# Kernel optimization log

Measured on AMD Instinct MI355X. Metric: run time of the kernel, lower is better.

Reference implementation:

```python
import jax, jax.numpy as jnp
import numpy as np

T, B, E, H = 256, 8, 512, 32
EXP = 512            # number of expanded (periodic-image) keys
SMOOTH = 20.0        # smooth_factor


def setup_inputs() -> dict:
    key = jax.random.key(0)
    ks = jax.random.split(key, 12)
    s = 1.0 / np.sqrt(E)
    return {
        "query": jax.random.normal(ks[0], (T, B, E), dtype=jnp.float32),
        "outcell_index": jax.random.randint(ks[1], (B, EXP), 0, T),
        "expand_mask": jax.random.bernoulli(ks[2], 0.1, (B, EXP)),
        "key_padding_mask": jax.random.bernoulli(ks[3], 0.1, (B, T)),
        "local_attention_weight": jax.random.uniform(ks[4], (B, T, T + EXP), dtype=jnp.float32),
        "Wq": jax.random.normal(ks[5], (E, E), dtype=jnp.float32) * s,
        "bq": jnp.zeros((E,), dtype=jnp.float32),
        "Wk": jax.random.normal(ks[6], (E, E), dtype=jnp.float32) * s,   # k_bias=False
        "Wv": jax.random.normal(ks[7], (E, E), dtype=jnp.float32) * s,
        "bv": jnp.zeros((E,), dtype=jnp.float32),
        "Wo": jax.random.normal(ks[8], (E, E), dtype=jnp.float32) * s,
        "bo": jnp.zeros((E,), dtype=jnp.float32),
    }


def reference(query, outcell_index, expand_mask, key_padding_mask,
              local_attention_weight, Wq, bq, Wk, Wv, bv, Wo, bo):
    t, b, e = query.shape
    hd = e // H
    # QKV projections (torch Linear: y = x @ W.T + b)
    q = jnp.einsum('tbe,fe->tbf', query, Wq) + bq
    k = jnp.einsum('tbe,fe->tbf', query, Wk)          # no k bias
    v = jnp.einsum('tbe,fe->tbf', query, Wv) + bv
    # PBC gather-expand K/V along the time axis
    oc = outcell_index.T[:, :, None]                  # [EXP, B, 1]
    k = jnp.concatenate([k, jnp.take_along_axis(k, oc, axis=0)], axis=0)  # [S,B,E]
    v = jnp.concatenate([v, jnp.take_along_axis(v, oc, axis=0)], axis=0)
    s_len = k.shape[0]
    # [len, B, E] -> [B, H, len, hd]
    qh = q.reshape(t, b, H, hd).transpose(1, 2, 0, 3)
    kh = k.reshape(s_len, b, H, hd).transpose(1, 2, 0, 3)
    vh = v.reshape(s_len, b, H, hd).transpose(1, 2, 0, 3)
    # NOTE: forward() never applies self.scaling in this path (faithful)
    scores = jnp.einsum('bhtd,bhsd->bhts', qh, kh)    # [B,H,T,S]
    law = local_attention_weight[:, None]             # [B,1,T,S]
    scores = (scores + SMOOTH) * law - SMOOTH         # smooth softmax
    kpm = jnp.concatenate([key_padding_mask, expand_mask], axis=1)  # [B,S]
    scores = jnp.where(kpm[:, None, None, :], -jnp.inf, scores)
    probs = jax.nn.softmax(scores, axis=-1)
    probs = probs * law                               # post-softmax reweight
    attn = jnp.einsum('bhts,bhsd->bhtd', probs, vh)   # [B,H,T,hd]
    attn = attn.transpose(2, 0, 1, 3).reshape(t, b, e)
    return jnp.einsum('tbe,fe->tbf', attn, Wo) + bo
```

## Files before the change

### kernel.cpp

```cpp
#include <hip/hip_runtime.h>
#include <stdint.h>

#define T_ 256
#define B_ 8
#define E_ 512
#define H_ 32
#define HD_ 16
#define EXP_ 512
#define S_ 768
#define M_ 2048
#define SMOOTH_ 20.0f
#define PSTR 40
#define VSTR 800
#define LOG2E_ 1.44269504f
#define MB0_  (-100.988655f)

typedef __attribute__((ext_vector_type(8)))  short bf16x8;
typedef __attribute__((ext_vector_type(4)))  float f32x4;
typedef __attribute__((ext_vector_type(16))) float f32x16;

__device__ __forceinline__ unsigned int pku(float a, float b)
{
    return ((__float_as_uint(a) + 0x8000u) >> 16) |
           ((__float_as_uint(b) + 0x8000u) & 0xFFFF0000u);
}
__device__ __forceinline__ ushort bf1(float a)
{
    unsigned int u = __float_as_uint(a);
    u = u + 0x7FFFu + ((u >> 16) & 1u);
    return (ushort)(u >> 16);
}

union U16 { uint4 u; bf16x8 v; };

__global__ __launch_bounds__(512, 4)
void qkv_attn_kernel(const float* __restrict__ X,
                     const float* __restrict__ Wq, const float* __restrict__ Wk,
                     const float* __restrict__ Wv,
                     const float* __restrict__ bq, const float* __restrict__ bv,
                     const float* __restrict__ LAW,
                     const int* __restrict__ kpm, const int* __restrict__ em,
                     const int* __restrict__ oc, ushort* __restrict__ Ab)
{
    __shared__ __align__(16) char raw[81920];
    ushort* Ks  = (ushort*)(raw);
    ushort* Vt  = (ushort*)(raw + 24576);
    ushort* Qi  = (ushort*)(raw + 50176);
    float*  msf = (float*) (raw + 58368);
    ushort* Pbb = (ushort*)(raw + 61440);
    ushort* As  = (ushort*)(raw);
    ushort* Bs  = (ushort*)(raw + 36864);
    ushort* Ob  = Qi;

    const int bh  = blockIdx.x;
    const int b   = bh >> 5;
    const int h   = bh & 31;
    const int tid = threadIdx.x;
    const int w   = tid >> 6;
    const int l   = tid & 63;

    const int r0 = tid >> 3;
    const int c8 = tid & 7;
    const float* Xc = &X[((size_t)r0 * 8 + b) * E_ + c8 * 8];

    const int wr = tid >> 3;
    const int wk = tid & 7;
    const float* Wsel = (wr < 16) ? Wq : (wr < 32 ? Wk : Wv);
    const float* Wr = &Wsel[((size_t)(h * 16 + (wr & 15))) * E_ + wk * 8];
    const bool wload = (tid < 384);

    ushort* Bxw = &Bs[wr * 72 + wk * 8];

    f32x4 acc[2][3];
#pragma unroll
    for (int i = 0; i < 2; ++i)
#pragma unroll
        for (int m = 0; m < 3; ++m)
            acc[i][m] = (f32x4){0.f, 0.f, 0.f, 0.f};

    float4 xp[4][2], wp[2];
#pragma unroll
    for (int k = 0; k < 4; ++k) {
        xp[k][0] = *(const float4*)&Xc[(size_t)k * 262144];
        xp[k][1] = *(const float4*)&Xc[(size_t)k * 262144 + 4];
    }
    if (wload) { wp[0] = *(const float4*)&Wr[0]; wp[1] = *(const float4*)&Wr[4]; }

    const int ln = l & 15;
    const int lg = l >> 4;

    for (int it = 0; it < 8; ++it) {
        __syncthreads();
#pragma unroll
        for (int k = 0; k < 4; ++k)
            *(uint4*)&As[(r0 + 64 * k) * 72 + c8 * 8] = make_uint4(
                pku(xp[k][0].x, xp[k][0].y), pku(xp[k][0].z, xp[k][0].w),
                pku(xp[k][1].x, xp[k][1].y), pku(xp[k][1].z, xp[k][1].w));
        if (wload)
            *(uint4*)&Bxw[0] = make_uint4(pku(wp[0].x, wp[0].y), pku(wp[0].z, wp[0].w),
                                          pku(wp[1].x, wp[1].y), pku(wp[1].z, wp[1].w));
        __syncthreads();
        if (it < 7) {
            Xc += 64;
#pragma unroll
            for (int k = 0; k < 4; ++k) {
                xp[k][0] = *(const float4*)&Xc[(size_t)k * 262144];
                xp[k][1] = *(const float4*)&Xc[(size_t)k * 262144 + 4];
            }
            if (wload) { Wr += 64; wp[0] = *(const float4*)&Wr[0]; wp[1] = *(const float4*)&Wr[4]; }
        }
#pragma unroll
        for (int kb = 0; kb < 2; ++kb) {
            bf16x8 af0 = *(const bf16x8*)&As[(32 * w + ln) * 72 + kb * 32 + lg * 8];
            bf16x8 af1 = *(const bf16x8*)&As[(32 * w + 16 + ln) * 72 + kb * 32 + lg * 8];
#pragma unroll
            for (int m = 0; m < 3; ++m) {
                bf16x8 bfm = *(const bf16x8*)&Bs[(m * 16 + ln) * 72 + kb * 32 + lg * 8];
                acc[0][m] = __builtin_amdgcn_mfma_f32_16x16x32_bf16(af0, bfm, acc[0][m], 0, 0, 0);
                acc[1][m] = __builtin_amdgcn_mfma_f32_16x16x32_bf16(af1, bfm, acc[1][m], 0, 0, 0);
            }
        }
    }

    __syncthreads();

    {
        const float bqv = bq[h * 16 + ln];
        const float bvv = bv[h * 16 + ln];
#pragma unroll
        for (int i = 0; i < 2; ++i)
#pragma unroll
            for (int r = 0; r < 4; ++r) {
                const int t = 32 * w + 16 * i + lg * 4 + r;
                Qi[t * 16 + ln]    = bf1(acc[i][0][r] + bqv);
                Ks[t * 16 + ln]    = bf1(acc[i][1][r]);
                Vt[ln * VSTR + t]  = bf1(acc[i][2][r] + bvv);
            }
    }
    __syncthreads();

    {
        const int j   = tid;
        const int src = oc[b * EXP_ + j];
        uint4 k0 = *(const uint4*)&Ks[src * 16];
        uint4 k1 = *(const uint4*)&Ks[src * 16 + 8];
        *(uint4*)&Ks[(T_ + j) * 16]     = k0;
        *(uint4*)&Ks[(T_ + j) * 16 + 8] = k1;
#pragma unroll
        for (int d = 0; d < 16; ++d)
            Vt[d * VSTR + T_ + j] = Vt[d * VSTR + src];

        const int s = tid;
        const int m = (s < T_) ? kpm[b * T_ + s] : em[b * EXP_ + (s - T_)];
        msf[s] = m ? -1.0e5f : MB0_;
        if (tid < 256) {
            const int s2 = 512 + tid;
            msf[s2] = em[b * EXP_ + (s2 - T_)] ? -1.0e5f : MB0_;
        }
    }
    __syncthreads();

    const int slane = l & 31;
    const int khalf = l >> 5;
    const int tl = l & 15;
    const int kg = l >> 4;

    bf16x8 qf = *(const bf16x8*)&Qi[(w * 32 + slane) * 16 + khalf * 8];

    const f32x16 zero16 = {0.f,0.f,0.f,0.f,0.f,0.f,0.f,0.f,
                           0.f,0.f,0.f,0.f,0.f,0.f,0.f,0.f};
    f32x4 o0 = {0.f, 0.f, 0.f, 0.f};
    f32x4 o1 = {0.f, 0.f, 0.f, 0.f};
    float zacc[16];
#pragma unroll
    for (int r = 0; r < 16; ++r) zacc[r] = 0.f;

    const float* lawb = &LAW[((size_t)b * T_ + w * 32 + khalf * 4) * S_ + slane];
    ushort* pw = &Pbb[w * 32 * PSTR + slane];
    ushort* pt = &Pbb[w * 32 * PSTR];
    float*  Zbw = (float*)pt;

    for (int i = 0; i < S_ / 32; ++i) {
        bf16x8 kf = *(const bf16x8*)&Ks[(i * 32 + slane) * 16 + khalf * 8];

        float lw[16];
        const float* lp = lawb + i * 32;
#pragma unroll
        for (int r = 0; r < 16; ++r)
            lw[r] = lp[(size_t)((r & 3) + 8 * (r >> 2)) * S_];

        f32x16 sc = __builtin_amdgcn_mfma_f32_32x32x16_bf16(qf, kf, zero16, 0, 0, 0);
        const float mb = msf[i * 32 + slane];

#pragma unroll
        for (int r = 0; r < 16; ++r) {
            const float lwK = lw[r] * LOG2E_;
            const float arg = __builtin_fmaf(sc[r], lwK,
                              __builtin_fmaf(lwK, SMOOTH_, mb));
            const float e = __builtin_amdgcn_exp2f(arg);
            zacc[r] += e;
            const float p = e * lw[r];
            pw[((r & 3) + 8 * (r >> 2) + 4 * khalf) * PSTR] =
                (ushort)((__float_as_uint(p) + 0x8000u) >> 16);
        }

        bf16x8 vf = *(const bf16x8*)&Vt[tl * VSTR + i * 32 + kg * 8];
        {
            const ushort* pr0 = &pt[(0 * 16 + tl) * PSTR + kg * 8];
            U16 u;
            uint2 a0 = *(const uint2*)pr0;
            uint2 a1 = *(const uint2*)(pr0 + 4);
            u.u = make_uint4(a0.x, a0.y, a1.x, a1.y);
            o0 = __builtin_amdgcn_mfma_f32_16x16x32_bf16(vf, u.v, o0, 0, 0, 0);
            const ushort* pr1 = &pt[(1 * 16 + tl) * PSTR + kg * 8];
            uint2 b0 = *(const uint2*)pr1;
            uint2 b1 = *(const uint2*)(pr1 + 4);
            u.u = make_uint4(b0.x, b0.y, b1.x, b1.y);
            o1 = __builtin_amdgcn_mfma_f32_16x16x32_bf16(vf, u.v, o1, 0, 0, 0);
        }
    }

#pragma unroll
    for (int m = 1; m < 32; m <<= 1) {
#pragma unroll
        for (int r = 0; r < 16; ++r)
            zacc[r] += __shfl_xor(zacc[r], m);
    }
    if (l == 0 || l == 32) {
#pragma unroll
        for (int r = 0; r < 16; ++r)
            Zbw[(r & 3) + 8 * (r >> 2) + 4 * khalf] = zacc[r];
    }
    __syncthreads();

#pragma unroll
    for (int th = 0; th < 2; ++th) {
        const int trow = th * 16 + tl;
        const float Zt  = Zbw[trow];
        const float inv = (Zt > 0.f) ? 1.f / Zt : 0.f;
        const f32x4 o = th ? o1 : o0;
        const int t = w * 32 + trow;
        *(uint*)&Ob[t * 16 + kg * 4]     = pku(o[0] * inv, o[1] * inv);
        *(uint*)&Ob[t * 16 + kg * 4 + 2] = pku(o[2] * inv, o[3] * inv);
    }
    __syncthreads();

    {
        ushort* dp = &Ab[((size_t)(b * H_ + h)) * T_ * HD_];
        *(uint4*)&dp[tid * 8] = *(const uint4*)&Ob[tid * 8];
    }
}

__device__ __forceinline__ void out_gemm_body(const ushort* __restrict__ Xh, int xstep,
                                              const float* __restrict__ Wf, int wstep,
                                              f32x4 acc[2][2],
                                              ushort* As, ushort* Bs)
{
    const int tid  = threadIdx.x;
    const int lrow = tid >> 2;
    const int kq   = tid & 3;
    const int l    = tid & 63;
    const int w    = tid >> 6;
    const int wm   = w & 1;
    const int wn   = w >> 1;
    const int lq   = l >> 4;
    const int ln   = l & 15;

    ushort* Aw = &As[lrow * 72 + kq * 16];
    ushort* Bw = &Bs[lrow * 72 + kq * 16];

    uint4  ha0 = *(const uint4*)&Xh[0];
    uint4  ha1 = *(const uint4*)&Xh[8];
    float4 fb0 = *(const float4*)&Wf[0];
    float4 fb1 = *(const float4*)&Wf[4];
    float4 fb2 = *(const float4*)&Wf[8];
    float4 fb3 = *(const float4*)&Wf[12];

    for (int it = 0; it < E_ / 64; ++it) {
        __syncthreads();
        *(uint4*)&Aw[0] = ha0;
        *(uint4*)&Aw[8] = ha1;
        *(uint4*)&Bw[0] = make_uint4(pku(fb0.x, fb0.y), pku(fb0.z, fb0.w),
                                     pku(fb1.x, fb1.y), pku(fb1.z, fb1.w));
        *(uint4*)&Bw[8] = make_uint4(pku(fb2.x, fb2.y), pku(fb2.z, fb2.w),
                                     pku(fb3.x, fb3.y), pku(fb3.z, fb3.w));
        __syncthreads();
        if (it < E_ / 64 - 1) {
            Xh += xstep;
            ha0 = *(const uint4*)&Xh[0];
            ha1 = *(const uint4*)&Xh[8];
            Wf += wstep;
            fb0 = *(const float4*)&Wf[0];
            fb1 = *(const float4*)&Wf[4];
            fb2 = *(const float4*)&Wf[8];
            fb3 = *(const float4*)&Wf[12];
        }
#pragma unroll
        for (int kb = 0; kb < 2; ++kb) {
            bf16x8 af0 = *(const bf16x8*)&As[(32 * wm + ln) * 72 + 32 * kb + lq * 8];
            bf16x8 af1 = *(const bf16x8*)&As[(32 * wm + 16 + ln) * 72 + 32 * kb + lq * 8];
            bf16x8 bf0 = *(const bf16x8*)&Bs[(32 * wn + ln) * 72 + 32 * kb + lq * 8];
            bf16x8 bf1 = *(const bf16x8*)&Bs[(32 * wn + 16 + ln) * 72 + 32 * kb + lq * 8];
            acc[0][0] = __builtin_amdgcn_mfma_f32_16x16x32_bf16(af0, bf0, acc[0][0], 0, 0, 0);
            acc[0][1] = __builtin_amdgcn_mfma_f32_16x16x32_bf16(af0, bf1, acc[0][1], 0, 0, 0);
            acc[1][0] = __builtin_amdgcn_mfma_f32_16x16x32_bf16(af1, bf0, acc[1][0], 0, 0, 0);
            acc[1][1] = __builtin_amdgcn_mfma_f32_16x16x32_bf16(af1, bf1, acc[1][1], 0, 0, 0);
        }
    }
}

__global__ __launch_bounds__(256)
void out_gemm(const ushort* __restrict__ Ab, const float* __restrict__ Wo,
              const float* __restrict__ bo, float* __restrict__ dst)
{
    __shared__ __align__(16) ushort AsBs[2 * 64 * 72];
    ushort* As = AsBs;
    ushort* Bs = AsBs + 64 * 72;

    const int m0 = blockIdx.y * 64;
    const int n0 = blockIdx.x * 64;

    f32x4 acc[2][2];
#pragma unroll
    for (int i = 0; i < 2; ++i)
#pragma unroll
        for (int j = 0; j < 2; ++j)
            acc[i][j] = (f32x4){0.f, 0.f, 0.f, 0.f};

    const int tid  = threadIdx.x;
    const int lrow = tid >> 2;
    const int kq   = tid & 3;
    const int m    = m0 + lrow;
    const int t    = m >> 3;
    const int b    = m & 7;
    out_gemm_body(&Ab[(((size_t)(b * H_ + kq)) * T_ + t) * HD_], 4 * T_ * HD_,
                  &Wo[(size_t)(n0 + lrow) * E_ + kq * 16], 64,
                  acc, As, Bs);

    const int l  = tid & 63;
    const int w  = tid >> 6;
    const int wm = w & 1;
    const int wn = w >> 1;
    const int lq = l >> 4;
    const int ln = l & 15;

    const float bo0 = bo[n0 + 32 * wn + ln];
    const float bo1 = bo[n0 + 32 * wn + 16 + ln];

    __syncthreads();
    float* Lf = (float*)AsBs;
#pragma unroll
    for (int j = 0; j < 2; ++j) {
        const float bb = j ? bo1 : bo0;
#pragma unroll
        for (int i = 0; i < 2; ++i)
#pragma unroll
            for (int r = 0; r < 4; ++r)
                Lf[(32 * wm + 16 * i + lq * 4 + r) * 68 + 32 * wn + 16 * j + ln] =
                    acc[i][j][r] + bb;
    }
    __syncthreads();

    {
        const int lm = tid & 63;
        const int hh = tid >> 6;
        float* dp = &dst[(size_t)(m0 + lm) * E_ + n0 + hh * 16];
#pragma unroll
        for (int c = 0; c < 4; ++c) {
            float4 v = *(const float4*)&Lf[lm * 68 + hh * 16 + c * 4];
            *(float4*)&dp[c * 4] = v;
        }
    }
}

extern "C" void kernel_launch(void* const* d_in, const int* in_sizes, int n_in,
                              void* d_out, int out_size, void* d_ws, size_t ws_size,
                              hipStream_t stream)
{
    const float* query = (const float*)d_in[0];
    const int*   oc    = (const int*)d_in[1];
    const int*   em    = (const int*)d_in[2];
    const int*   kpm   = (const int*)d_in[3];
    const float* law   = (const float*)d_in[4];
    const float* Wq    = (const float*)d_in[5];
    const float* bq    = (const float*)d_in[6];
    const float* Wk    = (const float*)d_in[7];
    const float* Wv    = (const float*)d_in[8];
    const float* bv    = (const float*)d_in[9];
    const float* Wo    = (const float*)d_in[10];
    const float* bo    = (const float*)d_in[11];
    float* out = (float*)d_out;

    ushort* Ab = (ushort*)d_ws;

    qkv_attn_kernel<<<B_ * H_, 512, 0, stream>>>(query, Wq, Wk, Wv, bq, bv,
                                                 law, kpm, em, oc, Ab);

    dim3 go(E_ / 64, M_ / 64, 1);
    out_gemm<<<go, 256, 0, stream>>>(Ab, Wo, bo, out);
}
```

Measured before the change: 129.1 us.

## Double attention block to 1024 threads, split key range and reduce partials

The fused QKV+attention kernel now launches 1024 threads per (batch, head). The projection gives each wave 16 rows, and the attention loop is split so two groups of waves each cover half of the 768 keys. Their partial outputs and softmax denominators are combined through LDS. The intermediate attention buffer is also written in [t,b,e] row-major layout, so the output GEMM reads contiguous rows instead of strided per-head chunks. This adds latency hiding and parallelism at the cost of more LDS (100KB), an extra reduction sync, and lower occupancy.

```diff
diff --git a/kernel.cpp b/kernel.cpp
--- a/kernel.cpp
+++ b/kernel.cpp
@@ -12,6 +12,7 @@
 #define SMOOTH_ 20.0f
 #define PSTR 40
 #define VSTR 800
+#define OSTR 20
 #define LOG2E_ 1.44269504f
 #define MB0_  (-100.988655f)
 
@@ -33,7 +34,7 @@
 
 union U16 { uint4 u; bf16x8 v; };
 
-__global__ __launch_bounds__(512, 4)
+__global__ __launch_bounds__(1024, 4)
 void qkv_attn_kernel(const float* __restrict__ X,
                      const float* __restrict__ Wq, const float* __restrict__ Wk,
                      const float* __restrict__ Wv,
@@ -42,7 +43,7 @@
                      const int* __restrict__ kpm, const int* __restrict__ em,
                      const int* __restrict__ oc, ushort* __restrict__ Ab)
 {
-    __shared__ __align__(16) char raw[81920];
+    __shared__ __align__(16) char raw[102400];
     ushort* Ks  = (ushort*)(raw);
     ushort* Vt  = (ushort*)(raw + 24576);
     ushort* Qi  = (ushort*)(raw + 50176);
@@ -50,6 +51,8 @@
     ushort* Pbb = (ushort*)(raw + 61440);
     ushort* As  = (ushort*)(raw);
     ushort* Bs  = (ushort*)(raw + 36864);
+    float*  Obuf= (float*) (raw);
+    float*  Zb  = (float*) (raw + 58368);
     ushort* Ob  = Qi;
 
     const int bh  = blockIdx.x;
@@ -61,63 +64,52 @@
 
     const int r0 = tid >> 3;
     const int c8 = tid & 7;
-    const float* Xc = &X[((size_t)r0 * 8 + b) * E_ + c8 * 8];
+    const float* Xc0 = &X[((size_t)r0 * 8 + b) * E_ + c8 * 8];
+    const float* Xc1 = Xc0 + (size_t)128 * 8 * E_;
 
     const int wr = tid >> 3;
-    const int wk = tid & 7;
+    const bool wload = (tid < 384);
     const float* Wsel = (wr < 16) ? Wq : (wr < 32 ? Wk : Wv);
-    const float* Wr = &Wsel[((size_t)(h * 16 + (wr & 15))) * E_ + wk * 8];
-    const bool wload = (tid < 384);
-
-    ushort* Bxw = &Bs[wr * 72 + wk * 8];
-
-    f32x4 acc[2][3];
-#pragma unroll
-    for (int i = 0; i < 2; ++i)
-#pragma unroll
-        for (int m = 0; m < 3; ++m)
-            acc[i][m] = (f32x4){0.f, 0.f, 0.f, 0.f};
-
-    float4 xp[4][2], wp[2];
-#pragma unroll
-    for (int k = 0; k < 4; ++k) {
-        xp[k][0] = *(const float4*)&Xc[(size_t)k * 262144];
-        xp[k][1] = *(const float4*)&Xc[(size_t)k * 262144 + 4];
-    }
-    if (wload) { wp[0] = *(const float4*)&Wr[0]; wp[1] = *(const float4*)&Wr[4]; }
+    const float* Wr = &Wsel[((size_t)(h * 16 + (wr & 15))) * E_ + c8 * 8];
+    ushort* Bxw = &Bs[wr * 72 + c8 * 8];
+
+    f32x4 acc[3];
+#pragma unroll
+    for (int m = 0; m < 3; ++m) acc[m] = (f32x4){0.f, 0.f, 0.f, 0.f};
+
+    float4 xa0, xa1, xb0, xb1, wp0, wp1;
+    xa0 = *(const float4*)&Xc0[0]; xa1 = *(const float4*)&Xc0[4];
+    xb0 = *(const float4*)&Xc1[0]; xb1 = *(const float4*)&Xc1[4];
+    if (wload) { wp0 = *(const float4*)&Wr[0]; wp1 = *(const float4*)&Wr[4]; }
 
     const int ln = l & 15;
     const int lg = l >> 4;
 
     for (int it = 0; it < 8; ++it) {
         __syncthreads();
-#pragma unroll
-        for (int k = 0; k < 4; ++k)
-            *(uint4*)&As[(r0 + 64 * k) * 72 + c8 * 8] = make_uint4(
-                pku(xp[k][0].x, xp[k][0].y), pku(xp[k][0].z, xp[k][0].w),
-                pku(xp[k][1].x, xp[k][1].y), pku(xp[k][1].z, xp[k][1].w));
+        *(uint4*)&As[r0 * 72 + c8 * 8] =
+            make_uint4(pku(xa0.x, xa0.y), pku(xa0.z, xa0.w),
+                       pku(xa1.x, xa1.y), pku(xa1.z, xa1.w));
+        *(uint4*)&As[(r0 + 128) * 72 + c8 * 8] =
+            make_uint4(pku(xb0.x, xb0.y), pku(xb0.z, xb0.w),
+                       pku(xb1.x, xb1.y), pku(xb1.z, xb1.w));
         if (wload)
-            *(uint4*)&Bxw[0] = make_uint4(pku(wp[0].x, wp[0].y), pku(wp[0].z, wp[0].w),
-                                          pku(wp[1].x, wp[1].y), pku(wp[1].z, wp[1].w));
+            *(uint4*)&Bxw[0] = make_uint4(pku(wp0.x, wp0.y), pku(wp0.z, wp0.w),
+                                          pku(wp1.x, wp1.y), pku(wp1.z, wp1.w));
         __syncthreads();
         if (it < 7) {
-            Xc += 64;
-#pragma unroll
-            for (int k = 0; k < 4; ++k) {
-                xp[k][0] = *(const float4*)&Xc[(size_t)k * 262144];
-                xp[k][1] = *(const float4*)&Xc[(size_t)k * 262144 + 4];
-            }
-            if (wload) { Wr += 64; wp[0] = *(const float4*)&Wr[0]; wp[1] = *(const float4*)&Wr[4]; }
+            Xc0 += 64; Xc1 += 64;
+            xa0 = *(const float4*)&Xc0[0]; xa1 = *(const float4*)&Xc0[4];
+            xb0 = *(const float4*)&Xc1[0]; xb1 = *(const float4*)&Xc1[4];
+            if (wload) { Wr += 64; wp0 = *(const float4*)&Wr[0]; wp1 = *(const float4*)&Wr[4]; }
         }
 #pragma unroll
         for (int kb = 0; kb < 2; ++kb) {
-            bf16x8 af0 = *(const bf16x8*)&As[(32 * w + ln) * 72 + kb * 32 + lg * 8];
-            bf16x8 af1 = *(const bf16x8*)&As[(32 * w + 16 + ln) * 72 + kb * 32 + lg * 8];
+            bf16x8 af = *(const bf16x8*)&As[(w * 16 + ln) * 72 + kb * 32 + lg * 8];
 #pragma unroll
             for (int m = 0; m < 3; ++m) {
                 bf16x8 bfm = *(const bf16x8*)&Bs[(m * 16 + ln) * 72 + kb * 32 + lg * 8];
-                acc[0][m] = __builtin_amdgcn_mfma_f32_16x16x32_bf16(af0, bfm, acc[0][m], 0, 0, 0);
-                acc[1][m] = __builtin_amdgcn_mfma_f32_16x16x32_bf16(af1, bfm, acc[1][m], 0, 0, 0);
+                acc[m] = __builtin_amdgcn_mfma_f32_16x16x32_bf16(af, bfm, acc[m], 0, 0, 0);
             }
         }
     }
@@ -128,35 +120,33 @@
         const float bqv = bq[h * 16 + ln];
         const float bvv = bv[h * 16 + ln];
 #pragma unroll
-        for (int i = 0; i < 2; ++i)
-#pragma unroll
-            for (int r = 0; r < 4; ++r) {
-                const int t = 32 * w + 16 * i + lg * 4 + r;
-                Qi[t * 16 + ln]    = bf1(acc[i][0][r] + bqv);
-                Ks[t * 16 + ln]    = bf1(acc[i][1][r]);
-                Vt[ln * VSTR + t]  = bf1(acc[i][2][r] + bvv);
-            }
-    }
-    __syncthreads();
-
-    {
+        for (int r = 0; r < 4; ++r) {
+            const int t = w * 16 + lg * 4 + r;
+            Qi[t * 16 + ln]   = bf1(acc[0][r] + bqv);
+            Ks[t * 16 + ln]   = bf1(acc[1][r]);
+            Vt[ln * VSTR + t] = bf1(acc[2][r] + bvv);
+        }
+    }
+    __syncthreads();
+
+    if (tid < 512) {
         const int j   = tid;
         const int src = oc[b * EXP_ + j];
         uint4 k0 = *(const uint4*)&Ks[src * 16];
         uint4 k1 = *(const uint4*)&Ks[src * 16 + 8];
         *(uint4*)&Ks[(T_ + j) * 16]     = k0;
         *(uint4*)&Ks[(T_ + j) * 16 + 8] = k1;
+    } else {
+        const int j   = tid - 512;
+        const int src = oc[b * EXP_ + j];
 #pragma unroll
         for (int d = 0; d < 16; ++d)
             Vt[d * VSTR + T_ + j] = Vt[d * VSTR + src];
-
+    }
+    if (tid < 768) {
         const int s = tid;
         const int m = (s < T_) ? kpm[b * T_ + s] : em[b * EXP_ + (s - T_)];
         msf[s] = m ? -1.0e5f : MB0_;
-        if (tid < 256) {
-            const int s2 = 512 + tid;
-            msf[s2] = em[b * EXP_ + (s2 - T_)] ? -1.0e5f : MB0_;
-        }
     }
     __syncthreads();
 
@@ -164,8 +154,10 @@
     const int khalf = l >> 5;
     const int tl = l & 15;
     const int kg = l >> 4;
-
-    bf16x8 qf = *(const bf16x8*)&Qi[(w * 32 + slane) * 16 + khalf * 8];
+    const int tq = w & 7;
+    const int sh = w >> 3;
+
+    bf16x8 qf = *(const bf16x8*)&Qi[(tq * 32 + slane) * 16 + khalf * 8];
 
     const f32x16 zero16 = {0.f,0.f,0.f,0.f,0.f,0.f,0.f,0.f,
                            0.f,0.f,0.f,0.f,0.f,0.f,0.f,0.f};
@@ -175,12 +167,11 @@
 #pragma unroll
     for (int r = 0; r < 16; ++r) zacc[r] = 0.f;
 
-    const float* lawb = &LAW[((size_t)b * T_ + w * 32 + khalf * 4) * S_ + slane];
+    const float* lawb = &LAW[((size_t)b * T_ + tq * 32 + khalf * 4) * S_ + slane];
     ushort* pw = &Pbb[w * 32 * PSTR + slane];
     ushort* pt = &Pbb[w * 32 * PSTR];
-    float*  Zbw = (float*)pt;
-
-    for (int i = 0; i < S_ / 32; ++i) {
+
+    for (int i = sh * 12; i < sh * 12 + 12; ++i) {
         bf16x8 kf = *(const bf16x8*)&Ks[(i * 32 + slane) * 16 + khalf * 8];
 
         float lw[16];
@@ -226,33 +217,50 @@
         for (int r = 0; r < 16; ++r)
             zacc[r] += __shfl_xor(zacc[r], m);
     }
+
+    __syncthreads();
+
     if (l == 0 || l == 32) {
 #pragma unroll
         for (int r = 0; r < 16; ++r)
-            Zbw[(r & 3) + 8 * (r >> 2) + 4 * khalf] = zacc[r];
-    }
-    __syncthreads();
-
-#pragma unroll
-    for (int th = 0; th < 2; ++th) {
-        const int trow = th * 16 + tl;
-        const float Zt  = Zbw[trow];
-        const float inv = (Zt > 0.f) ? 1.f / Zt : 0.f;
-        const f32x4 o = th ? o1 : o0;
-        const int t = w * 32 + trow;
-        *(uint*)&Ob[t * 16 + kg * 4]     = pku(o[0] * inv, o[1] * inv);
-        *(uint*)&Ob[t * 16 + kg * 4 + 2] = pku(o[2] * inv, o[3] * inv);
+            Zb[sh * 256 + tq * 32 + (r & 3) + 8 * (r >> 2) + 4 * khalf] = zacc[r];
+    }
+    if (sh == 1) {
+#pragma unroll
+        for (int th = 0; th < 2; ++th) {
+            const f32x4 o = th ? o1 : o0;
+            *(float4*)&Obuf[((size_t)(tq * 32 + th * 16 + tl)) * OSTR + kg * 4] =
+                make_float4(o[0], o[1], o[2], o[3]);
+        }
+    }
+    __syncthreads();
+
+    if (sh == 0) {
+#pragma unroll
+        for (int th = 0; th < 2; ++th) {
+            const int t = tq * 32 + th * 16 + tl;
+            const float Zt  = Zb[t] + Zb[256 + t];
+            const float inv = (Zt > 0.f) ? 1.f / Zt : 0.f;
+            float4 po = *(const float4*)&Obuf[(size_t)t * OSTR + kg * 4];
+            const f32x4 o = th ? o1 : o0;
+            float ov[4] = {(o[0] + po.x) * inv, (o[1] + po.y) * inv,
+                           (o[2] + po.z) * inv, (o[3] + po.w) * inv};
+            *(uint*)&Ob[t * 16 + kg * 4]     = pku(ov[0], ov[1]);
+            *(uint*)&Ob[t * 16 + kg * 4 + 2] = pku(ov[2], ov[3]);
+        }
     }
     __syncthreads();
 
     {
-        ushort* dp = &Ab[((size_t)(b * H_ + h)) * T_ * HD_];
-        *(uint4*)&dp[tid * 8] = *(const uint4*)&Ob[tid * 8];
-    }
-}
-
-__device__ __forceinline__ void out_gemm_body(const ushort* __restrict__ Xh, int xstep,
-                                              const float* __restrict__ Wf, int wstep,
+        const int t  = tid >> 2;
+        const int q4 = tid & 3;
+        *(uint2*)&Ab[((size_t)(t * 8 + b)) * E_ + h * 16 + q4 * 4] =
+            *(const uint2*)&Ob[t * 16 + q4 * 4];
+    }
+}
+
+__device__ __forceinline__ void out_gemm_body(const ushort* __restrict__ Xh,
+                                              const float* __restrict__ Wf,
                                               f32x4 acc[2][2],
                                               ushort* As, ushort* Bs)
 {
@@ -286,10 +294,10 @@
                                      pku(fb3.x, fb3.y), pku(fb3.z, fb3.w));
         __syncthreads();
         if (it < E_ / 64 - 1) {
-            Xh += xstep;
+            Xh += 64;
             ha0 = *(const uint4*)&Xh[0];
             ha1 = *(const uint4*)&Xh[8];
-            Wf += wstep;
+            Wf += 64;
             fb0 = *(const float4*)&Wf[0];
             fb1 = *(const float4*)&Wf[4];
             fb2 = *(const float4*)&Wf[8];
@@ -330,11 +338,8 @@
     const int tid  = threadIdx.x;
     const int lrow = tid >> 2;
     const int kq   = tid & 3;
-    const int m    = m0 + lrow;
-    const int t    = m >> 3;
-    const int b    = m & 7;
-    out_gemm_body(&Ab[(((size_t)(b * H_ + kq)) * T_ + t) * HD_], 4 * T_ * HD_,
-                  &Wo[(size_t)(n0 + lrow) * E_ + kq * 16], 64,
+    out_gemm_body(&Ab[(size_t)(m0 + lrow) * E_ + kq * 16],
+                  &Wo[(size_t)(n0 + lrow) * E_ + kq * 16],
                   acc, As, Bs);
 
     const int l  = tid & 63;
@@ -393,8 +398,8 @@
 
     ushort* Ab = (ushort*)d_ws;
 
-    qkv_attn_kernel<<<B_ * H_, 512, 0, stream>>>(query, Wq, Wk, Wv, bq, bv,
-                                                 law, kpm, em, oc, Ab);
+    qkv_attn_kernel<<<B_ * H_, 1024, 0, stream>>>(query, Wq, Wk, Wv, bq, bv,
+                                                  law, kpm, em, oc, Ab);
 
     dim3 go(E_ / 64, M_ / 64, 1);
     out_gemm<<<go, 256, 0, stream>>>(Ab, Wo, bo, out);
```

Result: faster. 124.0 us (-4.0%).
